# Optimization experiments

Hardware: AMD Instinct MI355X
Metric: run time of the kernel (lower is better)

Reference implementation:

```python
import jax, jax.numpy as jnp
import numpy as np

FACTOR = 5  # sampling factor c

def setup_inputs() -> dict:
    key = jax.random.key(0)
    k1, k2, k3, k4 = jax.random.split(key, 4)
    B, H, L, D = 4, 8, 2048, 64
    u = min(max(1, FACTOR * int(np.ceil(np.log(L)))), L)  # sample_k = 40
    return {
        "queries": jax.random.normal(k1, (B, H, L, D), jnp.float32),
        "keys": jax.random.normal(k2, (B, H, L, D), jnp.float32),
        "values": jax.random.normal(k3, (B, H, L, D), jnp.float32),
        "index_sample": jax.random.randint(k4, (L, u), 0, L, jnp.int32),
    }

def reference(queries, keys, values, index_sample):
    B, H, L_Q, D = queries.shape
    L_K = keys.shape[2]
    scale = 1.0 / np.sqrt(D)
    U_part = min(max(1, FACTOR * int(np.ceil(np.log(L_K)))), L_Q)  # n_top queries

    # --- _prob_QK: sampled scores + sparsity measure ---
    # K_sample[b,h,q,s,:] = keys[b,h,index_sample[q,s],:]  -> (B,H,L_Q,u,D)
    K_sample = keys[:, :, index_sample, :]
    QK_sample = jnp.einsum('bhqd,bhqsd->bhqs', queries, K_sample)  # (B,H,L_Q,u)
    M = QK_sample.max(-1) - QK_sample.sum(-1) / L_K                # (B,H,L_Q)
    _, index = jax.lax.top_k(M, U_part)                            # (B,H,U)

    # --- initial context: mean of V for non-selected queries ---
    context = jnp.broadcast_to(values.mean(-2, keepdims=True), (B, H, L_Q, D))

    # --- full attention for the top-U queries only ---
    Q_reduce = jnp.take_along_axis(queries, index[..., None], axis=2)   # (B,H,U,D)
    scores = jnp.einsum('bhud,bhkd->bhuk', Q_reduce, keys) * scale      # (B,H,U,L_K)
    attn = jax.nn.softmax(scores, axis=-1)
    out = jnp.einsum('bhuk,bhkd->bhud', attn, values)                   # (B,H,U,D)

    # --- scatter selected outputs back into the mean context ---
    bi = jnp.arange(B)[:, None, None]
    hi = jnp.arange(H)[None, :, None]
    context = context.at[bi, hi, index].set(out)
    return context
```

## Files before the change

### kernel.cpp

```cpp
#include <hip/hip_runtime.h>
#include <math.h>

#define Bq 4
#define Hh 8
#define Lh 2048
#define Dh 64
#define BH (Bq*Hh)

__global__ __launch_bounds__(256) void kA_M(const float* __restrict__ Q,
                                            const float* __restrict__ K,
                                            const int* __restrict__ idxs,
                                            float* __restrict__ M, int u) {
    int bi = blockIdx.x;
    int xcd = bi & 7, slot = bi >> 3;
    int bh  = xcd * 4 + (slot >> 5);
    int qt  = slot & 31;
    int tid = threadIdx.x;
    int wave = tid >> 6, lane = tid & 63;
    int g = lane >> 2, c = lane & 3;
    int q = qt * 64 + wave * 16 + g;
    long gq = (long)bh * Lh + q;

    const float* qrow = Q + gq * Dh;
    float4 qf[4];
#pragma unroll
    for (int jj = 0; jj < 4; ++jj)
        qf[jj] = *(const float4*)(qrow + jj * 16 + c * 4);

    const float* kbase = K + (long)bh * Lh * Dh;
    const int* irow = idxs + q * u;
    float mx = -INFINITY, sm = 0.f;
    int s = 0;
    for (; s + 4 <= u; s += 4) {
        int4 ki = *(const int4*)(irow + s);
        {
            const float* k0 = kbase + (long)ki.x * Dh + c * 4;
            const float* k1 = kbase + (long)ki.y * Dh + c * 4;
            float4 kf0[4], kf1[4];
#pragma unroll
            for (int jj = 0; jj < 4; ++jj) { kf0[jj] = *(const float4*)(k0 + jj * 16);
                                             kf1[jj] = *(const float4*)(k1 + jj * 16); }
            float a0 = 0.f, a1 = 0.f;
#pragma unroll
            for (int jj = 0; jj < 4; ++jj) {
                a0 += qf[jj].x*kf0[jj].x + qf[jj].y*kf0[jj].y + qf[jj].z*kf0[jj].z + qf[jj].w*kf0[jj].w;
                a1 += qf[jj].x*kf1[jj].x + qf[jj].y*kf1[jj].y + qf[jj].z*kf1[jj].z + qf[jj].w*kf1[jj].w;
            }
            a0 += __shfl_xor(a0, 1); a0 += __shfl_xor(a0, 2);
            a1 += __shfl_xor(a1, 1); a1 += __shfl_xor(a1, 2);
            mx = fmaxf(mx, fmaxf(a0, a1)); sm += a0 + a1;
        }
        {
            const float* k0 = kbase + (long)ki.z * Dh + c * 4;
            const float* k1 = kbase + (long)ki.w * Dh + c * 4;
            float4 kf0[4], kf1[4];
#pragma unroll
            for (int jj = 0; jj < 4; ++jj) { kf0[jj] = *(const float4*)(k0 + jj * 16);
                                             kf1[jj] = *(const float4*)(k1 + jj * 16); }
            float a0 = 0.f, a1 = 0.f;
#pragma unroll
            for (int jj = 0; jj < 4; ++jj) {
                a0 += qf[jj].x*kf0[jj].x + qf[jj].y*kf0[jj].y + qf[jj].z*kf0[jj].z + qf[jj].w*kf0[jj].w;
                a1 += qf[jj].x*kf1[jj].x + qf[jj].y*kf1[jj].y + qf[jj].z*kf1[jj].z + qf[jj].w*kf1[jj].w;
            }
            a0 += __shfl_xor(a0, 1); a0 += __shfl_xor(a0, 2);
            a1 += __shfl_xor(a1, 1); a1 += __shfl_xor(a1, 2);
            mx = fmaxf(mx, fmaxf(a0, a1)); sm += a0 + a1;
        }
    }
    for (; s < u; ++s) {
        int ki = irow[s];
        const float* krow = kbase + (long)ki * Dh + c * 4;
        float acc = 0.f;
#pragma unroll
        for (int jj = 0; jj < 4; ++jj) {
            float4 kf = *(const float4*)(krow + jj * 16);
            acc += qf[jj].x*kf.x + qf[jj].y*kf.y + qf[jj].z*kf.z + qf[jj].w*kf.w;
        }
        acc += __shfl_xor(acc, 1);
        acc += __shfl_xor(acc, 2);
        mx = fmaxf(mx, acc); sm += acc;
    }
    if (c == 0) M[gq] = mx - sm * (1.0f / (float)Lh);
}

__global__ __launch_bounds__(256) void kB_topk(const float* __restrict__ M,
                                               int* __restrict__ topk, int U) {
    int bh = blockIdx.x, tid = threadIdx.x;
    const float* m = M + (long)bh * Lh;
    unsigned key[8];
#pragma unroll
    for (int j = 0; j < 8; ++j) {
        unsigned ub = __float_as_uint(m[tid + 256 * j]);
        key[j] = ub ^ ((ub >> 31) ? 0xFFFFFFFFu : 0x80000000u);
    }
    __shared__ unsigned hist[256];
    __shared__ unsigned prefix_s;
    __shared__ int need_s;
    if (tid == 0) { prefix_s = 0u; need_s = U; }

    for (int level = 3; level >= 0; --level) {
        int shift = level * 8;
        hist[tid] = 0u;
        __syncthreads();
        unsigned prefix = prefix_s;
        int need = need_s;
        unsigned pmask = (level == 3) ? 0u : (0xFFFFFFFFu << (shift + 8));
#pragma unroll
        for (int j = 0; j < 8; ++j)
            if ((key[j] & pmask) == prefix)
                atomicAdd(&hist[(key[j] >> shift) & 0xFF], 1u);
        __syncthreads();
        if (tid < 64) {
            int lane = tid;
            unsigned h0 = hist[lane*4+0], h1 = hist[lane*4+1],
                     h2 = hist[lane*4+2], h3 = hist[lane*4+3];
            unsigned lt = h0 + h1 + h2 + h3;
            unsigned ssum = lt;
#pragma unroll
            for (int off = 1; off < 64; off <<= 1) {
                unsigned t = __shfl_down(ssum, off);
                if (lane + off < 64) ssum += t;
            }
            unsigned sx  = ssum - lt;
            unsigned suf3 = sx  + h3;
            unsigned suf2 = suf3 + h2;
            unsigned suf1 = suf2 + h1;
            unsigned suf0 = suf1 + h0;
            int localb = -1; unsigned nxt = 0u;
            if      ((int)suf3 >= need) { localb = lane*4+3; nxt = sx;   }
            else if ((int)suf2 >= need) { localb = lane*4+2; nxt = suf3; }
            else if ((int)suf1 >= need) { localb = lane*4+1; nxt = suf2; }
            else if ((int)suf0 >= need) { localb = lane*4+0; nxt = suf1; }
            unsigned long long ball = __ballot(localb >= 0);
            int hilane = 63 - __clzll(ball);
            if (lane == hilane) {
                prefix_s = prefix | ((unsigned)localb << shift);
                need_s = need - (int)nxt;
            }
        }
        __syncthreads();
    }
    unsigned T = prefix_s;
    int r = need_s;
    __shared__ int cgt, ceq;
    if (tid == 0) { cgt = 0; ceq = 0; }
    __syncthreads();
    int* out = topk + bh * U;
#pragma unroll
    for (int j = 0; j < 8; ++j) {
        if (key[j] > T) { int p = atomicAdd(&cgt, 1); out[p] = tid + 256 * j; }
        else if (key[j] == T) { int e = atomicAdd(&ceq, 1); if (e < r) out[U - r + e] = tid + 256 * j; }
    }
}

__global__ __launch_bounds__(256) void kC_vpart(const float* __restrict__ V,
                                                float* __restrict__ vpart) {
    int bi = blockIdx.x;
    int xcd = bi & 7, slot = bi >> 3;
    int bh = xcd * 4 + (slot >> 3);
    int chunk = slot & 7;
    int tid = threadIdx.x;
    int d = tid & 63, r0 = tid >> 6;
    const float* vb = V + ((long)bh * Lh + chunk * 256) * Dh;
    float s = 0.f;
    for (int i = 0; i < 64; ++i) s += vb[(r0 + 4 * i) * Dh + d];
    __shared__ float part[4][64];
    part[r0][d] = s;
    __syncthreads();
    if (tid < 64) {
        float t = part[0][tid] + part[1][tid] + part[2][tid] + part[3][tid];
        vpart[(bh * 8 + chunk) * 64 + tid] = t;
    }
}

__global__ __launch_bounds__(256) void kE_fill(const float* __restrict__ vpart,
                                               float* __restrict__ ctx) {
    int tid = threadIdx.x;
    long base = (long)blockIdx.x * 1024;
    int bh = (int)(base >> 17);
    __shared__ float vm[64];
    if (tid < 64) {
        float s = 0.f;
#pragma unroll
        for (int c2 = 0; c2 < 8; ++c2) s += vpart[(bh * 8 + c2) * 64 + tid];
        vm[tid] = s * (1.0f / (float)Lh);
    }
    __syncthreads();
    float4 val = *(const float4*)(vm + ((tid * 4) & 63));
    *(float4*)(ctx + base + tid * 4) = val;
}

#define TK 64
__global__ __launch_bounds__(256) void kD_part(const float* __restrict__ Q,
                                               const float* __restrict__ K,
                                               const float* __restrict__ V,
                                               const int* __restrict__ topk,
                                               float* __restrict__ pm,
                                               float* __restrict__ pl,
                                               float* __restrict__ pacc,
                                               int U, int nch) {
    int bi = blockIdx.x;
    int xcd = bi & 7, slot = bi >> 3;
    int per = nch * 8;
    int bh = xcd * 4 + slot / per;
    int rest = slot % per;
    int uc = rest >> 3, kc = rest & 7;

    int tid = threadIdx.x;
    int wv = tid >> 6, lane = tid & 63;

    __shared__ float Qs[8 * 64];
    __shared__ float Ks[TK * 68];
    __shared__ float Vs[TK * 64];
    __shared__ float Ps[8 * 68];
    __shared__ float alph[8], mst[8], lst[8];
    __shared__ int   qidxs[8];
    float* accbuf = Ks;

    if (tid < 8) {
        int gu = uc * 8 + tid;
        qidxs[tid] = (gu < U) ? topk[bh * U + gu] : 0;
    }
    __syncthreads();
#pragma unroll
    for (int step = 0; step < 2; ++step) {
        int uu = step * 4 + wv;
        int row = qidxs[uu];
        Qs[uu * 64 + lane] = Q[((long)bh * Lh + row) * Dh + lane] * 0.125f;
    }
    __syncthreads();

    int kq = tid & 63;
    int ug = tid >> 6;
    float mrun0 = -INFINITY, mrun1 = -INFINITY;
    float lrun0 = 0.f, lrun1 = 0.f;
    int pu = (tid >> 4) & 7, pd4 = tid & 15, kh = tid >> 7;
    float4 acc = {0.f, 0.f, 0.f, 0.f};

    const long kvbase = (long)bh * Lh * Dh;
    const float4* Kg4 = (const float4*)(K + kvbase);
    const float4* Vg4 = (const float4*)(V + kvbase);
    int kbase0 = kc * 256;

    for (int t0 = 0; t0 < 256; t0 += TK) {
        int f40 = (kbase0 + t0) * (Dh / 4);
#pragma unroll
        for (int j = 0; j < 4; ++j) {
            int i = tid + 256 * j;
            float4 kv = Kg4[f40 + i];
            int row = i >> 4, col = i & 15;
            *(float4*)(&Ks[row * 68 + col * 4]) = kv;
            float4 vv = Vg4[f40 + i];
            *(float4*)(&Vs[i * 4]) = vv;
        }
        __syncthreads();

        float s0 = 0.f, s1 = 0.f;
#pragma unroll
        for (int j16 = 0; j16 < 16; ++j16) {
            float4 kf = *(const float4*)(&Ks[kq * 68 + j16 * 4]);
            float4 qa = *(const float4*)(&Qs[(2 * ug + 0) * 64 + j16 * 4]);
            float4 qb = *(const float4*)(&Qs[(2 * ug + 1) * 64 + j16 * 4]);
            s0 += kf.x * qa.x + kf.y * qa.y + kf.z * qa.z + kf.w * qa.w;
            s1 += kf.x * qb.x + kf.y * qb.y + kf.z * qb.z + kf.w * qb.w;
        }
        float m0 = s0, m1 = s1;
#pragma unroll
        for (int off = 1; off < 64; off <<= 1) {
            m0 = fmaxf(m0, __shfl_xor(m0, off));
            m1 = fmaxf(m1, __shfl_xor(m1, off));
        }
        float mn0 = fmaxf(mrun0, m0), mn1 = fmaxf(mrun1, m1);
        float a0 = __expf(mrun0 - mn0), a1 = __expf(mrun1 - mn1);
        float p0 = __expf(s0 - mn0),  p1 = __expf(s1 - mn1);
        float ls0 = p0, ls1 = p1;
#pragma unroll
        for (int off = 1; off < 64; off <<= 1) {
            ls0 += __shfl_xor(ls0, off);
            ls1 += __shfl_xor(ls1, off);
        }
        lrun0 = a0 * lrun0 + ls0;  lrun1 = a1 * lrun1 + ls1;
        mrun0 = mn0;               mrun1 = mn1;
        Ps[(2 * ug + 0) * 68 + kq] = p0;
        Ps[(2 * ug + 1) * 68 + kq] = p1;
        if (lane == 0) { alph[2 * ug] = a0; alph[2 * ug + 1] = a1; }
        __syncthreads();

        float av = alph[pu];
        acc.x *= av; acc.y *= av; acc.z *= av; acc.w *= av;
#pragma unroll
        for (int k4 = 0; k4 < 8; ++k4) {
            int kk = kh * 32 + k4 * 4;
            float4 pf = *(const float4*)(&Ps[pu * 68 + kk]);
            float4 v0 = *(const float4*)(&Vs[(kk + 0) * 64 + pd4 * 4]);
            float4 v1 = *(const float4*)(&Vs[(kk + 1) * 64 + pd4 * 4]);
            float4 v2 = *(const float4*)(&Vs[(kk + 2) * 64 + pd4 * 4]);
            float4 v3 = *(const float4*)(&Vs[(kk + 3) * 64 + pd4 * 4]);
            acc.x += pf.x * v0.x + pf.y * v1.x + pf.z * v2.x + pf.w * v3.x;
            acc.y += pf.x * v0.y + pf.y * v1.y + pf.z * v2.y + pf.w * v3.y;
            acc.z += pf.x * v0.z + pf.y * v1.z + pf.z * v2.z + pf.w * v3.z;
            acc.w += pf.x * v0.w + pf.y * v1.w + pf.z * v2.w + pf.w * v3.w;
        }
        __syncthreads();
    }

    if (lane == 0) {
        mst[2 * ug] = mrun0; lst[2 * ug] = lrun0;
        mst[2 * ug + 1] = mrun1; lst[2 * ug + 1] = lrun1;
    }
    *(float4*)(&accbuf[tid * 4]) = acc;
    __syncthreads();
    int pbase = ((bh * nch + uc) * 8);
    if (tid < 128) {
        int u = tid >> 4, d4 = tid & 15;
        float4 x0 = *(const float4*)(&accbuf[tid * 4]);
        float4 x1 = *(const float4*)(&accbuf[(tid + 128) * 4]);
        float4 o;
        o.x = x0.x + x1.x; o.y = x0.y + x1.y;
        o.z = x0.z + x1.z; o.w = x0.w + x1.w;
        *(float4*)(pacc + ((long)(pbase + u) * 8 + kc) * 64 + d4 * 4) = o;
    }
    if (tid < 8) {
        int qp = (pbase + tid) * 8 + kc;
        pm[qp] = mst[tid];
        pl[qp] = lst[tid];
    }
}

__global__ __launch_bounds__(256) void kF_comb(const float* __restrict__ pm,
                                               const float* __restrict__ pl,
                                               const float* __restrict__ pacc,
                                               const int* __restrict__ topk,
                                               float* __restrict__ ctx,
                                               int U, int nch) {
    int bi = blockIdx.x;
    int bh = bi / nch, uc = bi % nch;
    int tid = threadIdx.x;
    int u = tid >> 5, t = tid & 31;
    int gu = uc * 8 + u;
    if (gu >= U) return;
    int qbase = (bh * nch + uc) * 8 + u;
    float m[8], l[8];
#pragma unroll
    for (int kc = 0; kc < 8; ++kc) { m[kc] = pm[qbase * 8 + kc]; l[kc] = pl[qbase * 8 + kc]; }
    float gm = m[0];
#pragma unroll
    for (int kc = 1; kc < 8; ++kc) gm = fmaxf(gm, m[kc]);
    float w[8]; float gl = 0.f;
#pragma unroll
    for (int kc = 0; kc < 8; ++kc) { w[kc] = __expf(m[kc] - gm); gl += l[kc] * w[kc]; }
    float inv = 1.0f / gl;
    float o0 = 0.f, o1 = 0.f;
#pragma unroll
    for (int kc = 0; kc < 8; ++kc) {
        const float* a = pacc + ((long)qbase * 8 + kc) * 64;
        o0 += a[t] * w[kc];
        o1 += a[t + 32] * w[kc];
    }
    int row = topk[bh * U + gu];
    float* crow = ctx + ((long)bh * Lh + row) * Dh;
    crow[t]      = o0 * inv;
    crow[t + 32] = o1 * inv;
}

extern "C" void kernel_launch(void* const* d_in, const int* in_sizes, int n_in,
                              void* d_out, int out_size, void* d_ws, size_t ws_size,
                              hipStream_t stream) {
    const float* Q    = (const float*)d_in[0];
    const float* K    = (const float*)d_in[1];
    const float* V    = (const float*)d_in[2];
    const int*   idxs = (const int*)d_in[3];
    float* ctx = (float*)d_out;

    int u = in_sizes[3] / Lh;
    int U = u;
    int nch = (U + 7) / 8;

    float* wsf   = (float*)d_ws;
    float* M     = wsf;
    int*   topk  = (int*)(wsf + 65536);
    float* vpart = wsf + 65536 + 2048;
    float* pm    = wsf + 83968;
    float* pl    = pm + 32 * nch * 8 * 8;
    float* pacc  = pl + 32 * nch * 8 * 8;

    kA_M    <<<1024,           256, 0, stream>>>(Q, K, idxs, M, u);
    kC_vpart<<<256,            256, 0, stream>>>(V, vpart);
    kB_topk <<<BH,             256, 0, stream>>>(M, topk, U);
    kE_fill <<<4096,           256, 0, stream>>>(vpart, ctx);
    kD_part <<<BH * nch * 8,   256, 0, stream>>>(Q, K, V, topk, pm, pl, pacc, U, nch);
    kF_comb <<<BH * nch,       256, 0, stream>>>(pm, pl, pacc, topk, ctx, U, nch);
}
```

Baseline: 167.2 us.

## Prefetch next K/V tile into registers and restructure PV accumulation per wave

The attention kernel now loads the next K/V tile into registers while computing on the current tile in shared memory, so global latency overlaps compute. The PV product is reorganized so each wave owns a 16-key slice and accumulates all 8 queries per lane, with a cross-wave reduction at the end. The sampled-score kernel also issues all four gathered key loads before any arithmetic to raise memory-level parallelism. The cost is higher register pressure and an extra shared-memory reduction pass.

```diff
diff --git a/kernel.cpp b/kernel.cpp
--- a/kernel.cpp
+++ b/kernel.cpp
@@ -33,39 +33,33 @@
     int s = 0;
     for (; s + 4 <= u; s += 4) {
         int4 ki = *(const int4*)(irow + s);
-        {
-            const float* k0 = kbase + (long)ki.x * Dh + c * 4;
-            const float* k1 = kbase + (long)ki.y * Dh + c * 4;
-            float4 kf0[4], kf1[4];
-#pragma unroll
-            for (int jj = 0; jj < 4; ++jj) { kf0[jj] = *(const float4*)(k0 + jj * 16);
-                                             kf1[jj] = *(const float4*)(k1 + jj * 16); }
-            float a0 = 0.f, a1 = 0.f;
-#pragma unroll
-            for (int jj = 0; jj < 4; ++jj) {
-                a0 += qf[jj].x*kf0[jj].x + qf[jj].y*kf0[jj].y + qf[jj].z*kf0[jj].z + qf[jj].w*kf0[jj].w;
-                a1 += qf[jj].x*kf1[jj].x + qf[jj].y*kf1[jj].y + qf[jj].z*kf1[jj].z + qf[jj].w*kf1[jj].w;
-            }
-            a0 += __shfl_xor(a0, 1); a0 += __shfl_xor(a0, 2);
-            a1 += __shfl_xor(a1, 1); a1 += __shfl_xor(a1, 2);
-            mx = fmaxf(mx, fmaxf(a0, a1)); sm += a0 + a1;
-        }
-        {
-            const float* k0 = kbase + (long)ki.z * Dh + c * 4;
-            const float* k1 = kbase + (long)ki.w * Dh + c * 4;
-            float4 kf0[4], kf1[4];
-#pragma unroll
-            for (int jj = 0; jj < 4; ++jj) { kf0[jj] = *(const float4*)(k0 + jj * 16);
-                                             kf1[jj] = *(const float4*)(k1 + jj * 16); }
-            float a0 = 0.f, a1 = 0.f;
-#pragma unroll
-            for (int jj = 0; jj < 4; ++jj) {
-                a0 += qf[jj].x*kf0[jj].x + qf[jj].y*kf0[jj].y + qf[jj].z*kf0[jj].z + qf[jj].w*kf0[jj].w;
-                a1 += qf[jj].x*kf1[jj].x + qf[jj].y*kf1[jj].y + qf[jj].z*kf1[jj].z + qf[jj].w*kf1[jj].w;
-            }
-            a0 += __shfl_xor(a0, 1); a0 += __shfl_xor(a0, 2);
-            a1 += __shfl_xor(a1, 1); a1 += __shfl_xor(a1, 2);
-            mx = fmaxf(mx, fmaxf(a0, a1)); sm += a0 + a1;
+        const float* kp0 = kbase + (long)ki.x * Dh + c * 4;
+        const float* kp1 = kbase + (long)ki.y * Dh + c * 4;
+        const float* kp2 = kbase + (long)ki.z * Dh + c * 4;
+        const float* kp3 = kbase + (long)ki.w * Dh + c * 4;
+        float4 kf[4][4];
+#pragma unroll
+        for (int jj = 0; jj < 4; ++jj) {
+            kf[0][jj] = *(const float4*)(kp0 + jj * 16);
+            kf[1][jj] = *(const float4*)(kp1 + jj * 16);
+            kf[2][jj] = *(const float4*)(kp2 + jj * 16);
+            kf[3][jj] = *(const float4*)(kp3 + jj * 16);
+        }
+        float a[4];
+#pragma unroll
+        for (int r = 0; r < 4; ++r) {
+            float ac = 0.f;
+#pragma unroll
+            for (int jj = 0; jj < 4; ++jj)
+                ac += qf[jj].x*kf[r][jj].x + qf[jj].y*kf[r][jj].y
+                    + qf[jj].z*kf[r][jj].z + qf[jj].w*kf[r][jj].w;
+            a[r] = ac;
+        }
+#pragma unroll
+        for (int r = 0; r < 4; ++r) {
+            a[r] += __shfl_xor(a[r], 1);
+            a[r] += __shfl_xor(a[r], 2);
+            mx = fmaxf(mx, a[r]); sm += a[r];
         }
     }
     for (; s < u; ++s) {
@@ -229,33 +223,45 @@
         int row = qidxs[uu];
         Qs[uu * 64 + lane] = Q[((long)bh * Lh + row) * Dh + lane] * 0.125f;
     }
-    __syncthreads();
-
-    int kq = tid & 63;
-    int ug = tid >> 6;
+
+    int kq = lane, ug = wv;
     float mrun0 = -INFINITY, mrun1 = -INFINITY;
     float lrun0 = 0.f, lrun1 = 0.f;
-    int pu = (tid >> 4) & 7, pd4 = tid & 15, kh = tid >> 7;
-    float4 acc = {0.f, 0.f, 0.f, 0.f};
+    float accv[8] = {0.f,0.f,0.f,0.f,0.f,0.f,0.f,0.f};
 
     const long kvbase = (long)bh * Lh * Dh;
     const float4* Kg4 = (const float4*)(K + kvbase);
     const float4* Vg4 = (const float4*)(V + kvbase);
     int kbase0 = kc * 256;
 
-    for (int t0 = 0; t0 < 256; t0 += TK) {
-        int f40 = (kbase0 + t0) * (Dh / 4);
+    float4 kreg[4], vreg[4];
+    {
+        int f40 = kbase0 * (Dh / 4);
 #pragma unroll
         for (int j = 0; j < 4; ++j) {
             int i = tid + 256 * j;
-            float4 kv = Kg4[f40 + i];
-            int row = i >> 4, col = i & 15;
-            *(float4*)(&Ks[row * 68 + col * 4]) = kv;
-            float4 vv = Vg4[f40 + i];
-            *(float4*)(&Vs[i * 4]) = vv;
-        }
-        __syncthreads();
-
+            kreg[j] = Kg4[f40 + i];
+            vreg[j] = Vg4[f40 + i];
+        }
+    }
+#pragma unroll
+    for (int j = 0; j < 4; ++j) {
+        int i = tid + 256 * j, row = i >> 4, col = i & 15;
+        *(float4*)(&Ks[row * 68 + col * 4]) = kreg[j];
+        *(float4*)(&Vs[i * 4]) = vreg[j];
+    }
+    __syncthreads();
+
+    for (int t = 0; t < 4; ++t) {
+        if (t < 3) {
+            int f40 = (kbase0 + (t + 1) * TK) * (Dh / 4);
+#pragma unroll
+            for (int j = 0; j < 4; ++j) {
+                int i = tid + 256 * j;
+                kreg[j] = Kg4[f40 + i];
+                vreg[j] = Vg4[f40 + i];
+            }
+        }
         float s0 = 0.f, s1 = 0.f;
 #pragma unroll
         for (int j16 = 0; j16 < 16; ++j16) {
@@ -287,39 +293,58 @@
         if (lane == 0) { alph[2 * ug] = a0; alph[2 * ug + 1] = a1; }
         __syncthreads();
 
-        float av = alph[pu];
-        acc.x *= av; acc.y *= av; acc.z *= av; acc.w *= av;
-#pragma unroll
-        for (int k4 = 0; k4 < 8; ++k4) {
-            int kk = kh * 32 + k4 * 4;
-            float4 pf = *(const float4*)(&Ps[pu * 68 + kk]);
-            float4 v0 = *(const float4*)(&Vs[(kk + 0) * 64 + pd4 * 4]);
-            float4 v1 = *(const float4*)(&Vs[(kk + 1) * 64 + pd4 * 4]);
-            float4 v2 = *(const float4*)(&Vs[(kk + 2) * 64 + pd4 * 4]);
-            float4 v3 = *(const float4*)(&Vs[(kk + 3) * 64 + pd4 * 4]);
-            acc.x += pf.x * v0.x + pf.y * v1.x + pf.z * v2.x + pf.w * v3.x;
-            acc.y += pf.x * v0.y + pf.y * v1.y + pf.z * v2.y + pf.w * v3.y;
-            acc.z += pf.x * v0.z + pf.y * v1.z + pf.z * v2.z + pf.w * v3.z;
-            acc.w += pf.x * v0.w + pf.y * v1.w + pf.z * v2.w + pf.w * v3.w;
+        float vk[16];
+#pragma unroll
+        for (int k = 0; k < 16; ++k)
+            vk[k] = Vs[(wv * 16 + k) * 64 + lane];
+#pragma unroll
+        for (int u2 = 0; u2 < 8; ++u2) {
+            const float* pb = &Ps[u2 * 68 + wv * 16];
+            float4 pA = *(const float4*)(pb + 0);
+            float4 pB = *(const float4*)(pb + 4);
+            float4 pC = *(const float4*)(pb + 8);
+            float4 pD = *(const float4*)(pb + 12);
+            float av = alph[u2];
+            float ac = accv[u2] * av;
+            ac += pA.x*vk[0]  + pA.y*vk[1]  + pA.z*vk[2]  + pA.w*vk[3];
+            ac += pB.x*vk[4]  + pB.y*vk[5]  + pB.z*vk[6]  + pB.w*vk[7];
+            ac += pC.x*vk[8]  + pC.y*vk[9]  + pC.z*vk[10] + pC.w*vk[11];
+            ac += pD.x*vk[12] + pD.y*vk[13] + pD.z*vk[14] + pD.w*vk[15];
+            accv[u2] = ac;
         }
         __syncthreads();
+
+        if (t < 3) {
+#pragma unroll
+            for (int j = 0; j < 4; ++j) {
+                int i = tid + 256 * j, row = i >> 4, col = i & 15;
+                *(float4*)(&Ks[row * 68 + col * 4]) = kreg[j];
+                *(float4*)(&Vs[i * 4]) = vreg[j];
+            }
+            __syncthreads();
+        }
     }
 
     if (lane == 0) {
-        mst[2 * ug] = mrun0; lst[2 * ug] = lrun0;
+        mst[2 * ug] = mrun0;     lst[2 * ug] = lrun0;
         mst[2 * ug + 1] = mrun1; lst[2 * ug + 1] = lrun1;
     }
-    *(float4*)(&accbuf[tid * 4]) = acc;
-    __syncthreads();
-    int pbase = ((bh * nch + uc) * 8);
-    if (tid < 128) {
-        int u = tid >> 4, d4 = tid & 15;
-        float4 x0 = *(const float4*)(&accbuf[tid * 4]);
-        float4 x1 = *(const float4*)(&accbuf[(tid + 128) * 4]);
-        float4 o;
-        o.x = x0.x + x1.x; o.y = x0.y + x1.y;
-        o.z = x0.z + x1.z; o.w = x0.w + x1.w;
-        *(float4*)(pacc + ((long)(pbase + u) * 8 + kc) * 64 + d4 * 4) = o;
+    __syncthreads();
+#pragma unroll
+    for (int u2 = 0; u2 < 8; ++u2)
+        accbuf[wv * 512 + u2 * 64 + lane] = accv[u2];
+    __syncthreads();
+
+    int pbase = (bh * nch + uc) * 8;
+    {
+        int d = tid & 63, ua = tid >> 6;
+#pragma unroll
+        for (int h = 0; h < 2; ++h) {
+            int u2 = ua + 4 * h;
+            float o = accbuf[0 * 512 + u2 * 64 + d] + accbuf[1 * 512 + u2 * 64 + d]
+                    + accbuf[2 * 512 + u2 * 64 + d] + accbuf[3 * 512 + u2 * 64 + d];
+            pacc[((long)(pbase + u2) * 8 + kc) * 64 + d] = o;
+        }
     }
     if (tid < 8) {
         int qp = (pbase + tid) * 8 + kc;
```

After: 194.8 us. +16.5%, slower.
